# Kernel optimization log

Measured on AMD Instinct MI355X. Metric: run time of the kernel, lower is better.

## Reference

```python
import jax, jax.numpy as jnp
import numpy as np

# Dimensions (match init_kwargs / input_specs)
B, C, H, W = 16, 16, 64, 64
N = H * W          # num_nodes
D_E = 64           # node_embed_dim
D_H = 128          # gnn_hidden_dim
D_R = 256          # readout_output_dim


def _param(key, shape, fan_in):
    return jax.random.normal(key, shape, jnp.float32) * (1.0 / np.sqrt(fan_in))


def setup_inputs() -> dict:
    key = jax.random.key(0)
    ks = jax.random.split(key, 16)
    inp = {
        "obs": jax.random.normal(ks[0], (B, C, H, W), jnp.float32),
        # node_embedding MLP (2 layers: C -> D_E -> D_E)
        "e1_w": _param(ks[1], (C, D_E), C),   "e1_b": jnp.zeros((D_E,), jnp.float32),
        "e2_w": _param(ks[2], (D_E, D_E), D_E), "e2_b": jnp.zeros((D_E,), jnp.float32),
        # 3 GNN layers (Linear then adjacency aggregation)
        "g1_w": _param(ks[3], (D_E, D_H), D_E), "g1_b": jnp.zeros((D_H,), jnp.float32),
        "g2_w": _param(ks[4], (D_H, D_H), D_H), "g2_b": jnp.zeros((D_H,), jnp.float32),
        "g3_w": _param(ks[5], (D_H, D_H), D_H), "g3_b": jnp.zeros((D_H,), jnp.float32),
        # readout MLP (2 layers: D_H -> 2*D_H -> D_R)
        "r1_w": _param(ks[6], (D_H, 2 * D_H), D_H),   "r1_b": jnp.zeros((2 * D_H,), jnp.float32),
        "r2_w": _param(ks[7], (2 * D_H, D_R), 2 * D_H), "r2_b": jnp.zeros((D_R,), jnp.float32),
    }
    return inp


def _adj_norm():
    # 4-neighbor grid adjacency on an H x W grid, row-normalized (same for every
    # batch element, so build once as (N, N) instead of (B, N, N)).
    idx = jnp.arange(N)
    up = jnp.eye(N, k=-W, dtype=jnp.float32)                      # i > 0
    down = jnp.eye(N, k=W, dtype=jnp.float32)                     # i < H-1
    left = jnp.eye(N, k=-1, dtype=jnp.float32) * ((idx % W) != 0)[:, None]
    right = jnp.eye(N, k=1, dtype=jnp.float32) * ((idx % W) != (W - 1))[:, None]
    adj = up + down + left + right
    return adj / (adj.sum(axis=1, keepdims=True) + 1e-6)


def reference(obs, e1_w, e1_b, e2_w, e2_b,
              g1_w, g1_b, g2_w, g2_b, g3_w, g3_b,
              r1_w, r1_b, r2_w, r2_b):
    relu = jax.nn.relu
    # grid -> graph: (B, C, H, W) -> (B, N, C)
    x = jnp.transpose(obs, (0, 2, 3, 1)).reshape(B, N, C)
    # node embedding MLP (output activation per ding MLP default)
    h = relu(x @ e1_w + e1_b)
    h = relu(h @ e2_w + e2_b)
    A = _adj_norm()  # (N, N)
    for Wg, bg in ((g1_w, g1_b), (g2_w, g2_b), (g3_w, g3_b)):
        support = h @ Wg + bg                      # (B, N, D_H)
        h = relu(jnp.einsum('nm,bmf->bnf', A, support))
    g = h.mean(axis=1)                              # (B, D_H) graph readout
    g = relu(g @ r1_w + r1_b)
    return relu(g @ r2_w + r2_b)                    # (B, D_R)
```

## Files before the change

kernel.cpp:

```cpp
#include <hip/hip_runtime.h>


typedef __attribute__((ext_vector_type(8))) short bf16x8;
typedef __attribute__((ext_vector_type(4))) float f32x4;
#define MFMA(a, b, c) __builtin_amdgcn_mfma_f32_16x16x32_bf16(a, b, c, 0, 0, 0)

__device__ inline ushort bf16h(float x) {
    unsigned u = __float_as_uint(x);
    return (ushort)((u + 0x7fffu + ((u >> 16) & 1u)) >> 16);
}
__device__ inline void split_bf16(float x, ushort& hi, ushort& lo) {
    hi = bf16h(x);
    lo = bf16h(x - __uint_as_float(((unsigned)hi) << 16));
}
__device__ inline unsigned pack_split(float x) {
    unsigned u = __float_as_uint(x);
    unsigned hi = (u + 0x7fffu + ((u >> 16) & 1u)) >> 16;
    float r = x - __uint_as_float(hi << 16);
    return (hi << 16) | (__float_as_uint(r) >> 16);
}
__device__ inline void frag_packed(const unsigned* bp, bf16x8& bh, bf16x8& bl) {
    unsigned p[8];
#pragma unroll
    for (int j = 0; j < 8; j++) p[j] = bp[j * 65];
    union { bf16x8 v; unsigned d[4]; } H, L;
#pragma unroll
    for (int j = 0; j < 4; j++) {
        const unsigned e = p[2 * j], o = p[2 * j + 1];
        H.d[j] = (o & 0xFFFF0000u) | (e >> 16);
        L.d[j] = (o << 16) | (e & 0xFFFFu);
    }
    bh = H.v; bl = L.v;
}

__global__ __launch_bounds__(64) void wprep_kernel(
    const float* __restrict__ e1w, const float* __restrict__ e2w,
    const float* __restrict__ g1w, const float* __restrict__ g2w,
    const float* __restrict__ g3w, ushort* __restrict__ wf,
    float* __restrict__ gsum)
{
    const int blk = blockIdx.x, l = threadIdx.x;
    if (blk >= 92) {
        gsum[(blk - 92) * 64 + l] = 0.f;
        return;
    }
    const float* src; int K, N, kc, t; ushort* dst;
    if (blk < 4)        { src = e1w; K = 16;  N = 64;  kc = 0; t = blk;      dst = wf; }
    else if (blk < 12)  { src = e2w; K = 64;  N = 64;  int u = blk - 4;  kc = u >> 2; t = u & 3; dst = wf + 4096; }
    else if (blk < 28)  { src = g1w; K = 64;  N = 128; int u = blk - 12; kc = u >> 3; t = u & 7; dst = wf + 12288; }
    else if (blk < 60)  { src = g2w; K = 128; N = 128; int u = blk - 28; kc = u >> 3; t = u & 7; dst = wf + 28672; }
    else                { src = g3w; K = 128; N = 128; int u = blk - 60; kc = u >> 3; t = u & 7; dst = wf + 61440; }
    const int T = (N == 64) ? 4 : 8;
    ushort* uh = dst + ((kc * T + t) * 2 + 0) * 512 + l * 8;
    ushort* ul = dst + ((kc * T + t) * 2 + 1) * 512 + l * 8;
    const int f = t * 16 + (l & 15);
    const int kb = kc * 32 + ((l >> 4) << 3);
#pragma unroll
    for (int j = 0; j < 8; j++) {
        const int k = kb + j;
        const float w = (k < K) ? src[k * N + f] : 0.f;
        ushort hi, lo; split_bf16(w, hi, lo);
        uh[j] = hi; ul[j] = lo;
    }
}

__global__ __launch_bounds__(256, 4) void embed_kernel(
    const float* __restrict__ obs, const ushort* __restrict__ wf,
    const float* __restrict__ e1b, const float* __restrict__ e2b,
    float* __restrict__ h0)
{
    __shared__ unsigned Xs[32 * 65];
    __shared__ unsigned Hs[64 * 65];
    const int tid = threadIdx.x, b = blockIdx.x >> 6, row = blockIdx.x & 63;
    const int lane = tid & 63, w = tid >> 6, quad = lane >> 4, nl = lane & 15;
    const int cp = tid >> 4, nq = tid & 15;

    const float4 x4 = *(const float4*)(obs + ((size_t)(b * 16 + cp) << 12) + row * 64 + nq * 4);
    unsigned* xp = Xs + cp * 65 + nq * 4;
    xp[0] = pack_split(x4.x); xp[1] = pack_split(x4.y);
    xp[2] = pack_split(x4.z); xp[3] = pack_split(x4.w);
    unsigned* zp = Xs + (16 + cp) * 65 + nq * 4;
    zp[0] = 0u; zp[1] = 0u; zp[2] = 0u; zp[3] = 0u;
    __syncthreads();

    {
        const ushort* wp = wf + lane * 8;
        const bf16x8 wh = *(const bf16x8*)(wp + (w * 2) * 512);
        const bf16x8 wl = *(const bf16x8*)(wp + (w * 2 + 1) * 512);
#pragma unroll
        for (int nt = 0; nt < 4; nt++) {
            const unsigned* bp = Xs + (quad * 8) * 65 + nt * 16 + nl;
            bf16x8 bh, bl; frag_packed(bp, bh, bl);
            f32x4 c = {0.f, 0.f, 0.f, 0.f};
            c = MFMA(wh, bh, c); c = MFMA(wh, bl, c); c = MFMA(wl, bh, c);
#pragma unroll
            for (int reg = 0; reg < 4; reg++) {
                const int fm = 16 * w + quad * 4 + reg;
                Hs[fm * 65 + nt * 16 + nl] = pack_split(fmaxf(c[reg] + e1b[fm], 0.f));
            }
        }
    }
    __syncthreads();

    const ushort* e2f = wf + 4096;
    f32x4 a2[4];
#pragma unroll
    for (int nt = 0; nt < 4; nt++) a2[nt] = (f32x4){0.f, 0.f, 0.f, 0.f};
#pragma unroll
    for (int kc = 0; kc < 2; kc++) {
        const ushort* wp = e2f + lane * 8;
        const bf16x8 wh = *(const bf16x8*)(wp + ((kc * 4 + w) * 2) * 512);
        const bf16x8 wl = *(const bf16x8*)(wp + ((kc * 4 + w) * 2 + 1) * 512);
#pragma unroll
        for (int nt = 0; nt < 4; nt++) {
            const unsigned* bp = Hs + (kc * 32 + quad * 8) * 65 + nt * 16 + nl;
            bf16x8 bh, bl; frag_packed(bp, bh, bl);
            a2[nt] = MFMA(wh, bh, a2[nt]);
            a2[nt] = MFMA(wh, bl, a2[nt]);
            a2[nt] = MFMA(wl, bh, a2[nt]);
        }
    }
#pragma unroll
    for (int reg = 0; reg < 4; reg++) {
        const int f = 16 * w + quad * 4 + reg;
        const float bv = e2b[f];
#pragma unroll
        for (int nt = 0; nt < 4; nt++)
            h0[((size_t)(b * 64 + f) << 12) + row * 64 + nt * 16 + nl] =
                fmaxf(a2[nt][reg] + bv, 0.f);
    }
}

template <int K, bool MEAN>
__global__ __launch_bounds__(256, 4) void gnn_kernel(
    const float* __restrict__ hin, const ushort* __restrict__ wf,
    const float* __restrict__ bias, float* __restrict__ hout,
    float* __restrict__ gsum)
{
    constexpr int NH = K / 64;
    __shared__ unsigned As[NH][64 * 65];
    const int tid = threadIdx.x;
    const int bid = ((blockIdx.x & 7) << 7) | (blockIdx.x >> 3);
    const int b = bid >> 6, row = bid & 63;
    const int lane = tid & 63, w = tid >> 6, quad = lane >> 4, nl = lane & 15;
    const int kp = tid >> 4, nq = tid & 15;
    const float* hb = hin + (size_t)b * K * 4096;
    const int rowu = (row > 0) ? row - 1 : row;
    const int rowd = (row < 63) ? row + 1 : row;
    const float su = (row > 0) ? 1.f : 0.f;
    const float sd = (row < 63) ? 1.f : 0.f;
    float inv[4];
#pragma unroll
    for (int i = 0; i < 4; i++) {
        const int n = nq * 4 + i;
        const int deg = (row > 0) + (row < 63) + (n > 0) + (n < 63);
        inv[i] = 1.f / ((float)deg + 1e-6f);
    }

    f32x4 acc[4][2];
#pragma unroll
    for (int nt = 0; nt < 4; nt++) {
        acc[nt][0] = (f32x4){0.f, 0.f, 0.f, 0.f};
        acc[nt][1] = (f32x4){0.f, 0.f, 0.f, 0.f};
    }

    auto load_group = [&](int kh, int it, float4& c, float4& u, float4& d) {
        const int kk = it * 16 + kp;
        const float* pk = hb + ((size_t)(kh * 64 + kk) << 12) + nq * 4;
        c = *(const float4*)(pk + row * 64);
        u = *(const float4*)(pk + rowu * 64);
        d = *(const float4*)(pk + rowd * 64);
    };
    auto stage_group = [&](int kh, int it, const float4& c, const float4& u, const float4& d) {
        const int kk = it * 16 + kp;
        const float pw = __shfl_up(c.w, 1);
        const float nx = __shfl_down(c.x, 1);
        const float lx = (nq > 0) ? pw : 0.f;
        const float rw = (nq < 15) ? nx : 0.f;
        unsigned* ap = As[kh] + kk * 65 + nq * 4;
        ap[0] = pack_split((su * u.x + sd * d.x + lx + c.y) * inv[0]);
        ap[1] = pack_split((su * u.y + sd * d.y + c.x + c.z) * inv[1]);
        ap[2] = pack_split((su * u.z + sd * d.z + c.y + c.w) * inv[2]);
        ap[3] = pack_split((su * u.w + sd * d.w + c.z + rw) * inv[3]);
    };
    auto load_stage_half = [&](int kh) {
        float4 c0, u0, d0, c1, u1, d1;
        load_group(kh, 0, c0, u0, d0);
        load_group(kh, 1, c1, u1, d1);
        stage_group(kh, 0, c0, u0, d0);
        load_group(kh, 2, c0, u0, d0);
        stage_group(kh, 1, c1, u1, d1);
        load_group(kh, 3, c1, u1, d1);
        stage_group(kh, 2, c0, u0, d0);
        stage_group(kh, 3, c1, u1, d1);
    };
    auto consume = [&](int kh) {
        const unsigned* src = As[kh];
#pragma unroll
        for (int kc = 0; kc < 2; kc++) {
            const int kcg = kh * 2 + kc;
            const ushort* wp = wf + lane * 8;
            const bf16x8 wh0 = *(const bf16x8*)(wp + ((kcg * 8 + 2 * w)     * 2)     * 512);
            const bf16x8 wl0 = *(const bf16x8*)(wp + ((kcg * 8 + 2 * w)     * 2 + 1) * 512);
            const bf16x8 wh1 = *(const bf16x8*)(wp + ((kcg * 8 + 2 * w + 1) * 2)     * 512);
            const bf16x8 wl1 = *(const bf16x8*)(wp + ((kcg * 8 + 2 * w + 1) * 2 + 1) * 512);
#pragma unroll
            for (int nt = 0; nt < 4; nt++) {
                const unsigned* bp = src + (kc * 32 + quad * 8) * 65 + nt * 16 + nl;
                bf16x8 bh, bl; frag_packed(bp, bh, bl);
                acc[nt][0] = MFMA(wh0, bh, acc[nt][0]);
                acc[nt][0] = MFMA(wh0, bl, acc[nt][0]);
                acc[nt][0] = MFMA(wl0, bh, acc[nt][0]);
                acc[nt][1] = MFMA(wh1, bh, acc[nt][1]);
                acc[nt][1] = MFMA(wh1, bl, acc[nt][1]);
                acc[nt][1] = MFMA(wl1, bh, acc[nt][1]);
            }
        }
    };

    load_stage_half(0);
    __syncthreads();
#pragma unroll
    for (int kh = 0; kh < NH; kh++) {
        if (kh + 1 < NH) load_stage_half(kh + 1);
        consume(kh);
        if (kh + 1 < NH) __syncthreads();
    }

    if (!MEAN) {
#pragma unroll
        for (int ftl = 0; ftl < 2; ftl++) {
            const int fb = 32 * w + 16 * ftl + quad * 4;
            const float b0 = bias[fb], b1 = bias[fb + 1], b2 = bias[fb + 2], b3 = bias[fb + 3];
#pragma unroll
            for (int nt = 0; nt < 4; nt++) {
                const int n = 16 * nt + nl;
                const int deg = (row > 0) + (row < 63) + (n > 0) + (n < 63);
                const float rs = (float)deg / ((float)deg + 1e-6f);
                float* op = hout + ((size_t)(b * 128 + fb) << 12) + row * 64 + n;
                op[0]        = fmaxf(acc[nt][ftl][0] + rs * b0, 0.f);
                op[1u << 12] = fmaxf(acc[nt][ftl][1] + rs * b1, 0.f);
                op[2u << 12] = fmaxf(acc[nt][ftl][2] + rs * b2, 0.f);
                op[3u << 12] = fmaxf(acc[nt][ftl][3] + rs * b3, 0.f);
            }
        }
    } else {
#pragma unroll
        for (int ftl = 0; ftl < 2; ftl++) {
            const int fb = 32 * w + 16 * ftl + quad * 4;
#pragma unroll
            for (int reg = 0; reg < 4; reg++) {
                const float bv = bias[fb + reg];
                float v = 0.f;
#pragma unroll
                for (int nt = 0; nt < 4; nt++) {
                    const int n = 16 * nt + nl;
                    const int deg = (row > 0) + (row < 63) + (n > 0) + (n < 63);
                    const float rs = (float)deg / ((float)deg + 1e-6f);
                    v += fmaxf(acc[nt][ftl][reg] + rs * bv, 0.f);
                }
                v += __shfl_xor(v, 1); v += __shfl_xor(v, 2);
                v += __shfl_xor(v, 4); v += __shfl_xor(v, 8);
                if (nl == 0) atomicAdd(&gsum[b * 128 + fb + reg], v * (1.f / 4096.f));
            }
        }
    }
}

__global__ __launch_bounds__(256) void readout_kernel(
    const float* __restrict__ gsum, const float* __restrict__ r1w,
    const float* __restrict__ r1b, const float* __restrict__ r2w,
    const float* __restrict__ r2b, float* __restrict__ out)
{
    __shared__ float gs[128];
    __shared__ float g2[256];
    const int b = blockIdx.x, tid = threadIdx.x;
    if (tid < 128) gs[tid] = gsum[b * 128 + tid];
    __syncthreads();
    float a = r1b[tid];
#pragma unroll 16
    for (int k = 0; k < 128; k++) a = fmaf(gs[k], r1w[k * 256 + tid], a);
    g2[tid] = fmaxf(a, 0.f);
    __syncthreads();
    float a2 = r2b[tid];
#pragma unroll 16
    for (int k = 0; k < 256; k++) a2 = fmaf(g2[k], r2w[k * 256 + tid], a2);
    out[b * 256 + tid] = fmaxf(a2, 0.f);
}

extern "C" void kernel_launch(void* const* d_in, const int* in_sizes, int n_in,
                              void* d_out, int out_size, void* d_ws, size_t ws_size,
                              hipStream_t stream)
{
    const float* obs = (const float*)d_in[0];
    const float* e1w = (const float*)d_in[1];
    const float* e1b = (const float*)d_in[2];
    const float* e2w = (const float*)d_in[3];
    const float* e2b = (const float*)d_in[4];
    const float* g1w = (const float*)d_in[5];
    const float* g1b = (const float*)d_in[6];
    const float* g2w = (const float*)d_in[7];
    const float* g2b = (const float*)d_in[8];
    const float* g3w = (const float*)d_in[9];
    const float* g3b = (const float*)d_in[10];
    const float* r1w = (const float*)d_in[11];
    const float* r1b = (const float*)d_in[12];
    const float* r2w = (const float*)d_in[13];
    const float* r2b = (const float*)d_in[14];
    float* out = (float*)d_out;
    float* ws = (float*)d_ws;

    float* h0 = ws;
    float* h1 = ws + 4194304;
    float* h2 = ws + 4194304 + 8388608;
    float* gsum = (float*)((char*)d_ws + 80u * 1024u * 1024u);
    ushort* wfb = (ushort*)((char*)d_ws + 80u * 1024u * 1024u + 8192u);

    hipLaunchKernelGGL(wprep_kernel, dim3(124), dim3(64), 0, stream,
                       e1w, e2w, g1w, g2w, g3w, wfb, gsum);
    hipLaunchKernelGGL(embed_kernel, dim3(1024), dim3(256), 0, stream,
                       obs, wfb, e1b, e2b, h0);
    hipLaunchKernelGGL((gnn_kernel<64, false>), dim3(1024), dim3(256), 0, stream,
                       h0, wfb + 12288, g1b, h1, nullptr);
    hipLaunchKernelGGL((gnn_kernel<128, false>), dim3(1024), dim3(256), 0, stream,
                       h1, wfb + 28672, g2b, h2, nullptr);
    hipLaunchKernelGGL((gnn_kernel<128, true>), dim3(1024), dim3(256), 0, stream,
                       h2, wfb + 61440, g3b, nullptr, gsum);
    hipLaunchKernelGGL(readout_kernel, dim3(16), dim3(256), 0, stream,
                       gsum, r1w, r1b, r2w, r2b, out);
}
```

Before: 163.1 us.

## Stage GNN input rows into LDS via async global_load_lds and preload weights

Replaces register-staged global loads of the up/center/down rows with direct global-to-LDS async loads (global_load_lds) into a raw buffer, then transforms that buffer into the packed split-bf16 operand tile. The next half's loads are issued right after the transform so they overlap with the MFMA work, and the weight fragments are hoisted into registers once before the loop. Occupancy hint drops from 4 to 2 blocks per CU because of the larger LDS footprint (raw 48KB plus As) and the extra weight registers, which risks less latency hiding. The added barriers and a transform-then-consume order may serialize part of the work.

```diff
diff --git a/kernel.cpp b/kernel.cpp
--- a/kernel.cpp
+++ b/kernel.cpp
@@ -4,6 +4,13 @@
 typedef __attribute__((ext_vector_type(8))) short bf16x8;
 typedef __attribute__((ext_vector_type(4))) float f32x4;
 #define MFMA(a, b, c) __builtin_amdgcn_mfma_f32_16x16x32_bf16(a, b, c, 0, 0, 0)
+#define WAIT_VM0() __builtin_amdgcn_s_waitcnt(0x0F70)
+
+__device__ inline void gll16(const float* g, float* l) {
+    __builtin_amdgcn_global_load_lds(
+        (const __attribute__((address_space(1))) void*)g,
+        (__attribute__((address_space(3))) void*)l, 16, 0, 0);
+}
 
 __device__ inline ushort bf16h(float x) {
     unsigned u = __float_as_uint(x);
@@ -132,13 +139,14 @@
 }
 
 template <int K, bool MEAN>
-__global__ __launch_bounds__(256, 4) void gnn_kernel(
+__global__ __launch_bounds__(256, 2) void gnn_kernel(
     const float* __restrict__ hin, const ushort* __restrict__ wf,
     const float* __restrict__ bias, float* __restrict__ hout,
     float* __restrict__ gsum)
 {
     constexpr int NH = K / 64;
-    __shared__ unsigned As[NH][64 * 65];
+    __shared__ __align__(16) float raw[3 * 64 * 64];
+    __shared__ __align__(16) unsigned As[64 * 65];
     const int tid = threadIdx.x;
     const int bid = ((blockIdx.x & 7) << 7) | (blockIdx.x >> 3);
     const int b = bid >> 6, row = bid & 63;
@@ -157,6 +165,16 @@
         inv[i] = 1.f / ((float)deg + 1e-6f);
     }
 
+    const ushort* wfl = wf + lane * 8;
+    bf16x8 W[NH * 2][2][2];
+#pragma unroll
+    for (int kcg = 0; kcg < NH * 2; kcg++)
+#pragma unroll
+        for (int ftl = 0; ftl < 2; ftl++) {
+            W[kcg][ftl][0] = *(const bf16x8*)(wfl + ((kcg * 8 + 2 * w + ftl) * 2) * 512);
+            W[kcg][ftl][1] = *(const bf16x8*)(wfl + ((kcg * 8 + 2 * w + ftl) * 2 + 1) * 512);
+        }
+
     f32x4 acc[4][2];
 #pragma unroll
     for (int nt = 0; nt < 4; nt++) {
@@ -164,67 +182,64 @@
         acc[nt][1] = (f32x4){0.f, 0.f, 0.f, 0.f};
     }
 
-    auto load_group = [&](int kh, int it, float4& c, float4& u, float4& d) {
-        const int kk = it * 16 + kp;
-        const float* pk = hb + ((size_t)(kh * 64 + kk) << 12) + nq * 4;
-        c = *(const float4*)(pk + row * 64);
-        u = *(const float4*)(pk + rowu * 64);
-        d = *(const float4*)(pk + rowd * 64);
+    auto gll_half = [&](int kh) {
+#pragma unroll
+        for (int i = 0; i < 12; i++) {
+            const int idx = w * 12 + i;
+            const int r = idx >> 4, q = idx & 15;
+            const int rsel = (r == 0) ? rowu : ((r == 1) ? row : rowd);
+            const int p = q * 4 + (lane >> 4);
+            const float* g = hb + ((size_t)(kh * 64 + p) << 12) + rsel * 64 + (lane & 15) * 4;
+            float* l = raw + (r * 64 + q * 4) * 64;
+            gll16(g, l);
+        }
     };
-    auto stage_group = [&](int kh, int it, const float4& c, const float4& u, const float4& d) {
-        const int kk = it * 16 + kp;
-        const float pw = __shfl_up(c.w, 1);
-        const float nx = __shfl_down(c.x, 1);
-        const float lx = (nq > 0) ? pw : 0.f;
-        const float rw = (nq < 15) ? nx : 0.f;
-        unsigned* ap = As[kh] + kk * 65 + nq * 4;
-        ap[0] = pack_split((su * u.x + sd * d.x + lx + c.y) * inv[0]);
-        ap[1] = pack_split((su * u.y + sd * d.y + c.x + c.z) * inv[1]);
-        ap[2] = pack_split((su * u.z + sd * d.z + c.y + c.w) * inv[2]);
-        ap[3] = pack_split((su * u.w + sd * d.w + c.z + rw) * inv[3]);
+    auto transform = [&]() {
+#pragma unroll
+        for (int it = 0; it < 4; it++) {
+            const int kk = it * 16 + kp;
+            const float4 u4 = *(const float4*)(raw + (0 * 64 + kk) * 64 + nq * 4);
+            const float4 c4 = *(const float4*)(raw + (1 * 64 + kk) * 64 + nq * 4);
+            const float4 d4 = *(const float4*)(raw + (2 * 64 + kk) * 64 + nq * 4);
+            const float pw = __shfl_up(c4.w, 1);
+            const float nx = __shfl_down(c4.x, 1);
+            const float lx = (nq > 0) ? pw : 0.f;
+            const float rw = (nq < 15) ? nx : 0.f;
+            unsigned* ap = As + kk * 65 + nq * 4;
+            ap[0] = pack_split((su * u4.x + sd * d4.x + lx + c4.y) * inv[0]);
+            ap[1] = pack_split((su * u4.y + sd * d4.y + c4.x + c4.z) * inv[1]);
+            ap[2] = pack_split((su * u4.z + sd * d4.z + c4.y + c4.w) * inv[2]);
+            ap[3] = pack_split((su * u4.w + sd * d4.w + c4.z + rw) * inv[3]);
+        }
     };
-    auto load_stage_half = [&](int kh) {
-        float4 c0, u0, d0, c1, u1, d1;
-        load_group(kh, 0, c0, u0, d0);
-        load_group(kh, 1, c1, u1, d1);
-        stage_group(kh, 0, c0, u0, d0);
-        load_group(kh, 2, c0, u0, d0);
-        stage_group(kh, 1, c1, u1, d1);
-        load_group(kh, 3, c1, u1, d1);
-        stage_group(kh, 2, c0, u0, d0);
-        stage_group(kh, 3, c1, u1, d1);
-    };
-    auto consume = [&](int kh) {
-        const unsigned* src = As[kh];
+
+    gll_half(0);
+    WAIT_VM0();
+    __syncthreads();
+#pragma unroll
+    for (int kh = 0; kh < NH; kh++) {
+        transform();
+        __syncthreads();
+        if (kh + 1 < NH) gll_half(kh + 1);
 #pragma unroll
         for (int kc = 0; kc < 2; kc++) {
             const int kcg = kh * 2 + kc;
-            const ushort* wp = wf + lane * 8;
-            const bf16x8 wh0 = *(const bf16x8*)(wp + ((kcg * 8 + 2 * w)     * 2)     * 512);
-            const bf16x8 wl0 = *(const bf16x8*)(wp + ((kcg * 8 + 2 * w)     * 2 + 1) * 512);
-            const bf16x8 wh1 = *(const bf16x8*)(wp + ((kcg * 8 + 2 * w + 1) * 2)     * 512);
-            const bf16x8 wl1 = *(const bf16x8*)(wp + ((kcg * 8 + 2 * w + 1) * 2 + 1) * 512);
 #pragma unroll
             for (int nt = 0; nt < 4; nt++) {
-                const unsigned* bp = src + (kc * 32 + quad * 8) * 65 + nt * 16 + nl;
+                const unsigned* bp = As + (kc * 32 + quad * 8) * 65 + nt * 16 + nl;
                 bf16x8 bh, bl; frag_packed(bp, bh, bl);
-                acc[nt][0] = MFMA(wh0, bh, acc[nt][0]);
-                acc[nt][0] = MFMA(wh0, bl, acc[nt][0]);
-                acc[nt][0] = MFMA(wl0, bh, acc[nt][0]);
-                acc[nt][1] = MFMA(wh1, bh, acc[nt][1]);
-                acc[nt][1] = MFMA(wh1, bl, acc[nt][1]);
-                acc[nt][1] = MFMA(wl1, bh, acc[nt][1]);
+                acc[nt][0] = MFMA(W[kcg][0][0], bh, acc[nt][0]);
+                acc[nt][0] = MFMA(W[kcg][0][0], bl, acc[nt][0]);
+                acc[nt][0] = MFMA(W[kcg][0][1], bh, acc[nt][0]);
+                acc[nt][1] = MFMA(W[kcg][1][0], bh, acc[nt][1]);
+                acc[nt][1] = MFMA(W[kcg][1][0], bl, acc[nt][1]);
+                acc[nt][1] = MFMA(W[kcg][1][1], bh, acc[nt][1]);
             }
         }
-    };
-
-    load_stage_half(0);
-    __syncthreads();
-#pragma unroll
-    for (int kh = 0; kh < NH; kh++) {
-        if (kh + 1 < NH) load_stage_half(kh + 1);
-        consume(kh);
-        if (kh + 1 < NH) __syncthreads();
+        if (kh + 1 < NH) {
+            WAIT_VM0();
+            __syncthreads();
+        }
     }
 
     if (!MEAN) {
```

Result: slower. 280.7 us (+72.1%).
